# Kernel tuning notes

Hardware: AMD Instinct MI355X
Metric: run time of the kernel (lower is better)

The kernel has to match this reference:

```python
import jax, jax.numpy as jnp
import numpy as np

ALPHA = 9.0
EPS = 2.220446049250313e-16  # sys.float_info.epsilon
N, K = 131072, 256


def setup_inputs() -> dict:
    key = jax.random.key(0)
    k1, k2 = jax.random.split(key)
    latent_view_1 = jax.random.uniform(k1, (N, K), dtype=jnp.float32)
    latent_view_2 = jax.random.uniform(k2, (N, K), dtype=jnp.float32)
    return {"latent_view_1": latent_view_1, "latent_view_2": latent_view_2}


def reference(latent_view_1, latent_view_2):
    # joint: sum_n v1[n,i] * v2[n,j]  == v1^T @ v2  (rank-N GEMM, [k,k] output)
    p_i_j = jnp.einsum('ni,nj->ij', latent_view_1, latent_view_2)
    p_i_j = (p_i_j + p_i_j.T) / 2.0
    p_i_j = p_i_j / jnp.sum(p_i_j)
    p_i = jnp.sum(p_i_j, axis=1, keepdims=True)  # [k,1] marginal
    p_j = jnp.sum(p_i_j, axis=0, keepdims=True)  # [1,k] marginal
    p_i_j = jnp.maximum(p_i_j, EPS)
    p_i = jnp.maximum(p_i, EPS)
    p_j = jnp.maximum(p_j, EPS)
    loss = -p_i_j * (jnp.log(p_i_j)
                     - (ALPHA + 1.0) * jnp.log(p_j)
                     - (ALPHA + 1.0) * jnp.log(p_i))
    return jnp.sum(loss)
```

## Files before the change

kernel.cpp:

```cpp
#include <hip/hip_runtime.h>
#include <hip/hip_bf16.h>

#define KDIM 256
#define NTOT 131072
#define PN   65536
#define NB   256
#define RPB  512
#define CHROWS 16
#define CH   (CHROWS*KDIM)
#define NTL  16

typedef float f32x4 __attribute__((ext_vector_type(4)));
typedef __bf16 bf16x8 __attribute__((ext_vector_type(8)));

__device__ __forceinline__ unsigned short f2bf(float x){
  unsigned u = __float_as_uint(x);
  u += 0x7fffu + ((u >> 16) & 1u);
  return (unsigned short)(u >> 16);
}
__device__ __forceinline__ unsigned pk2(float lo, float hi){
  return (unsigned)f2bf(lo) | ((unsigned)f2bf(hi) << 16);
}
__device__ __forceinline__ float bf2f(unsigned short u){
  return __uint_as_float((unsigned)u << 16);
}
__device__ __forceinline__ int swz(int i){ return (((i >> 1) ^ (i >> 4)) & 7) << 4; }

struct Stage { f32x4 r0, r1; };

__device__ __forceinline__ void stage_load(Stage& s, const float* src, long off){
  s.r0 = *(const f32x4*)(src + off);
  s.r1 = *(const f32x4*)(src + off + KDIM);
}

__device__ __forceinline__ void stage_store(const Stage& s, char* tile, const int* offW){
#pragma unroll
  for (int m = 0; m < 4; ++m)
    *(unsigned*)(tile + offW[m]) = pk2(s.r0[m], s.r1[m]);
}

__device__ __forceinline__ void compute_t(const char* As, const char* Bs,
                                          const int* offA, const int* offB,
                                          f32x4 (&acc)[4][4])
{
  bf16x8 af[4], bfr[4];
#pragma unroll
  for (int m = 0; m < 4; ++m) af[m]  = *(const bf16x8*)(As + offA[m]);
#pragma unroll
  for (int n = 0; n < 4; ++n) bfr[n] = *(const bf16x8*)(Bs + offB[n]);
#pragma unroll
  for (int m = 0; m < 4; ++m)
#pragma unroll
    for (int n = 0; n < 4; ++n)
      acc[m][n] = __builtin_amdgcn_mfma_f32_16x16x32_bf16(af[m], bfr[n], acc[m][n], 0, 0, 0);
}

__device__ __forceinline__ void lds_fence_barrier(){
  __builtin_amdgcn_sched_barrier(0);
  asm volatile("s_waitcnt lgkmcnt(0)");
  __builtin_amdgcn_sched_barrier(0);
  __builtin_amdgcn_s_barrier();
  __builtin_amdgcn_sched_barrier(0);
}

__global__ __launch_bounds__(1024) void k_gemm(const float* __restrict__ v1,
                                               const float* __restrict__ v2,
                                               unsigned short* __restrict__ part)
{
  __shared__ char sm[65536];
  const int t    = threadIdx.x;
  const int b    = blockIdx.x;
  const int lane = t & 63, wid = t >> 6;
  const int di   = lane & 15, g = lane >> 4;
  const int wr   = wid >> 2, wc = wid & 3;
  const int i0   = wr * 64, j0 = wc * 64;

  const int mtx = t >> 9;
  const int p   = (t >> 6) & 7;
  const int q   = t & 63;
  const float* src = (mtx ? v2 : v1) + ((long)b * RPB + 2 * p) * KDIM + 4 * q;
  const int sbase = mtx * 16384;

  int offW0[4], offW1[4], offA[4], offB[4];
#pragma unroll
  for (int m = 0; m < 4; ++m){
    const int i   = 4*q + m;
    const int lin = (i << 6) + (p << 2);
    offW0[m] = sbase + ( lin        ^ swz(i));
    offW1[m] = sbase + ((lin + 32)  ^ swz(i));
  }
#pragma unroll
  for (int m = 0; m < 4; ++m){ int i = i0 + 16*m + di; offA[m] = ((i << 6) + (g << 4)) ^ swz(i); }
#pragma unroll
  for (int n = 0; n < 4; ++n){ int j = j0 + 16*n + di; offB[n] = ((j << 6) + (g << 4)) ^ swz(j); }

  f32x4 acc[4][4];
#pragma unroll
  for (int m = 0; m < 4; ++m)
#pragma unroll
    for (int n = 0; n < 4; ++n){ f32x4 z = {0.f,0.f,0.f,0.f}; acc[m][n] = z; }

  Stage S0, S1;
  stage_load(S0, src, 0L * CH);
  stage_load(S1, src, 1L * CH);
  stage_store(S0, sm, offW0);
  __builtin_amdgcn_sched_barrier(0);
  stage_load(S0, src, 2L * CH);
  __builtin_amdgcn_sched_barrier(0);
  stage_store(S1, sm, offW1);
  __builtin_amdgcn_sched_barrier(0);
  stage_load(S1, src, 3L * CH);
  lds_fence_barrier();

#pragma unroll 2
  for (int it = 0; it < NTL - 2; ++it){
    char* Tc = sm + (it & 1) * 32768;
    char* Tn = sm + ((it + 1) & 1) * 32768;
    stage_store(S0, Tn, offW0);
    __builtin_amdgcn_sched_barrier(0);
    stage_load(S0, src, (long)(2*it + 4) * CH);
    __builtin_amdgcn_sched_barrier(0);
    stage_store(S1, Tn, offW1);
    __builtin_amdgcn_sched_barrier(0);
    stage_load(S1, src, (long)(2*it + 5) * CH);
    __builtin_amdgcn_sched_barrier(0);
    compute_t(Tc, Tc + 16384, offA, offB, acc);
    lds_fence_barrier();
  }

  {
    char* Tc = sm + ((NTL - 2) & 1) * 32768;
    char* Tn = sm + ((NTL - 1) & 1) * 32768;
    stage_store(S0, Tn, offW0);
    stage_store(S1, Tn, offW1);
    __builtin_amdgcn_sched_barrier(0);
    compute_t(Tc, Tc + 16384, offA, offB, acc);
    lds_fence_barrier();
    compute_t(Tn, Tn + 16384, offA, offB, acc);
  }

  unsigned short* op = part + (size_t)b * PN;
#pragma unroll
  for (int m = 0; m < 4; ++m)
#pragma unroll
    for (int n = 0; n < 4; ++n){
      const int i = i0 + 16*m + 4*g;
      const int j = j0 + 16*n + di;
#pragma unroll
      for (int r = 0; r < 4; ++r)
        op[(size_t)(i + r) * KDIM + j] = f2bf(acc[m][n][r]);
    }
}

__global__ __launch_bounds__(1024) void k_reduce(const unsigned short* __restrict__ part,
                                                 float* __restrict__ P,
                                                 float* __restrict__ rsum,
                                                 float* __restrict__ csum)
{
  __shared__ float red[1024];
  const int gr = blockIdx.x;
  const int t  = threadIdx.x;
  const int j  = t & 255, q = t >> 8;
  const int bpq = NB >> 2;
  float s = 0.f;
  const unsigned short* p = part + (size_t)(q * bpq) * PN + gr * KDIM + j;
  for (int b = 0; b < bpq; ++b) s += bf2f(p[(size_t)b * PN]);
  red[t] = s; __syncthreads();
  if (t < 512) red[t] += red[t + 512];
  __syncthreads();
  float v = 0.f;
  if (t < 256){
    v = red[t] + red[t + 256];
    P[gr * KDIM + t] = v;
    atomicAdd(&csum[t], v);
  }
  __syncthreads();
  red[t] = (t < 256) ? v : 0.f;
  __syncthreads();
  for (int st = 128; st > 0; st >>= 1){
    if (t < st) red[t] += red[t + st];
    __syncthreads();
  }
  if (t == 0) rsum[gr] = red[0];
}

__global__ __launch_bounds__(256) void k_marg(const float* __restrict__ rsum,
                                              const float* __restrict__ csum,
                                              float* __restrict__ lm,
                                              float* __restrict__ scal,
                                              float* __restrict__ out)
{
  __shared__ float red[256];
  const int i = threadIdx.x;
  float ri = rsum[i];
  red[i] = ri; __syncthreads();
  for (int st = 128; st > 0; st >>= 1){
    if (i < st) red[i] += red[i + st];
    __syncthreads();
  }
  const float S = red[0];
  const float inv2S = 0.5f / S;
  float mi = (ri + csum[i]) * inv2S;
  mi = fmaxf(mi, 2.220446049250313e-16f);
  lm[i] = logf(mi);
  if (i == 0){ scal[0] = inv2S; out[0] = 0.f; }
}

__global__ __launch_bounds__(256) void k_loss(const float* __restrict__ P,
                                              const float* __restrict__ lm,
                                              const float* __restrict__ scal,
                                              float* __restrict__ out)
{
  __shared__ float red[256];
  const float inv2S = scal[0];
  float acc = 0.f;
  const int base = blockIdx.x * 512;
  for (int e = base + threadIdx.x; e < base + 512; e += 256){
    const int i = e >> 8, j = e & 255;
    float q = (P[i * KDIM + j] + P[j * KDIM + i]) * inv2S;
    q = fmaxf(q, 2.220446049250313e-16f);
    acc += -q * (logf(q) - 10.0f * (lm[i] + lm[j]));
  }
  red[threadIdx.x] = acc; __syncthreads();
  for (int st = 128; st > 0; st >>= 1){
    if (threadIdx.x < st) red[threadIdx.x] += red[threadIdx.x + st];
    __syncthreads();
  }
  if (threadIdx.x == 0) atomicAdd(out, red[0]);
}

extern "C" void kernel_launch(void* const* d_in, const int* in_sizes, int n_in,
                              void* d_out, int out_size, void* d_ws, size_t ws_size,
                              hipStream_t stream) {
  const float* v1 = (const float*)d_in[0];
  const float* v2 = (const float*)d_in[1];
  float* out = (float*)d_out;
  char*  wsc = (char*)d_ws;

  unsigned short* part = (unsigned short*)wsc;
  float* P    = (float*)(wsc + (size_t)NB * PN * 2);
  float* rsum = P + PN;
  float* csum = rsum + 256;
  float* lm   = csum + 256;
  float* scal = lm + 256;

  hipMemsetAsync(csum, 0, 256 * sizeof(float), stream);
  k_gemm  <<<NB, 1024, 0, stream>>>(v1, v2, part);
  k_reduce<<<256, 1024, 0, stream>>>(part, P, rsum, csum);
  k_marg  <<<1, 256, 0, stream>>>(rsum, csum, lm, scal, out);
  k_loss  <<<128, 256, 0, stream>>>(P, lm, scal, out);
}
```

Measured before the change: 79.17 us.

## Split GEMM output columns across two 512-thread blocks with packed LDS offsets

The GEMM now launches 512 blocks of 512 threads, each computing a 256x128 half of the output instead of 256 blocks of 1024 threads computing the full 256x256. LDS use per block drops from 64KB to 48KB, and LDS offsets are packed into 16-bit pairs to save registers, with launch bounds asking for four blocks per CU. The goal is higher occupancy and better latency hiding. The cost is that every v1 row chunk is loaded twice, once per column half, and the reduce kernel's indexing changes to match the new partial-sum layout.

```diff
diff --git a/kernel.cpp b/kernel.cpp
--- a/kernel.cpp
+++ b/kernel.cpp
@@ -4,11 +4,12 @@
 #define KDIM 256
 #define NTOT 131072
 #define PN   65536
-#define NB   256
+#define NGB  512
 #define RPB  512
-#define CHROWS 16
-#define CH   (CHROWS*KDIM)
 #define NTL  16
+#define CH   (32*KDIM)
+#define PSZ  32768
+#define BUFB 24576
 
 typedef float f32x4 __attribute__((ext_vector_type(4)));
 typedef __bf16 bf16x8 __attribute__((ext_vector_type(8)));
@@ -33,26 +34,28 @@
   s.r1 = *(const f32x4*)(src + off + KDIM);
 }
 
-__device__ __forceinline__ void stage_store(const Stage& s, char* tile, const int* offW){
+__device__ __forceinline__ void stage_store(const Stage& s, char* T, const unsigned* pW, int x){
+#pragma unroll
+  for (int m = 0; m < 4; ++m){
+    const int off = (int)((pW[m >> 1] >> ((m & 1) * 16)) & 0xffffu) ^ x;
+    *(unsigned*)(T + off) = pk2(s.r0[m], s.r1[m]);
+  }
+}
+
+__device__ __forceinline__ void compute_t(const char* T, const unsigned* pFa,
+                                          const unsigned* pFb, f32x4 (&acc)[4][4])
+{
+  bf16x8 af[4];
 #pragma unroll
   for (int m = 0; m < 4; ++m)
-    *(unsigned*)(tile + offW[m]) = pk2(s.r0[m], s.r1[m]);
-}
-
-__device__ __forceinline__ void compute_t(const char* As, const char* Bs,
-                                          const int* offA, const int* offB,
-                                          f32x4 (&acc)[4][4])
-{
-  bf16x8 af[4], bfr[4];
-#pragma unroll
-  for (int m = 0; m < 4; ++m) af[m]  = *(const bf16x8*)(As + offA[m]);
-#pragma unroll
-  for (int n = 0; n < 4; ++n) bfr[n] = *(const bf16x8*)(Bs + offB[n]);
-#pragma unroll
-  for (int m = 0; m < 4; ++m)
-#pragma unroll
-    for (int n = 0; n < 4; ++n)
-      acc[m][n] = __builtin_amdgcn_mfma_f32_16x16x32_bf16(af[m], bfr[n], acc[m][n], 0, 0, 0);
+    af[m] = *(const bf16x8*)(T + ((pFa[m >> 1] >> ((m & 1) * 16)) & 0xffffu));
+#pragma unroll
+  for (int n = 0; n < 4; ++n){
+    bf16x8 bf = *(const bf16x8*)(T + ((pFb[n >> 1] >> ((n & 1) * 16)) & 0xffffu));
+#pragma unroll
+    for (int m = 0; m < 4; ++m)
+      acc[m][n] = __builtin_amdgcn_mfma_f32_16x16x32_bf16(af[m], bf, acc[m][n], 0, 0, 0);
+  }
 }
 
 __device__ __forceinline__ void lds_fence_barrier(){
@@ -63,36 +66,42 @@
   __builtin_amdgcn_sched_barrier(0);
 }
 
-__global__ __launch_bounds__(1024) void k_gemm(const float* __restrict__ v1,
-                                               const float* __restrict__ v2,
-                                               unsigned short* __restrict__ part)
-{
-  __shared__ char sm[65536];
+__global__ __launch_bounds__(512, 4) void k_gemm(const float* __restrict__ v1,
+                                                 const float* __restrict__ v2,
+                                                 unsigned short* __restrict__ part)
+{
+  __shared__ char sm[2 * BUFB];
   const int t    = threadIdx.x;
   const int b    = blockIdx.x;
+  const int r    = b & 255, h = b >> 8;
   const int lane = t & 63, wid = t >> 6;
   const int di   = lane & 15, g = lane >> 4;
-  const int wr   = wid >> 2, wc = wid & 3;
-  const int i0   = wr * 64, j0 = wc * 64;
-
-  const int mtx = t >> 9;
-  const int p   = (t >> 6) & 7;
-  const int q   = t & 63;
-  const float* src = (mtx ? v2 : v1) + ((long)b * RPB + 2 * p) * KDIM + 4 * q;
-  const int sbase = mtx * 16384;
-
-  int offW0[4], offW1[4], offA[4], offB[4];
-#pragma unroll
-  for (int m = 0; m < 4; ++m){
-    const int i   = 4*q + m;
-    const int lin = (i << 6) + (p << 2);
-    offW0[m] = sbase + ( lin        ^ swz(i));
-    offW1[m] = sbase + ((lin + 32)  ^ swz(i));
-  }
-#pragma unroll
-  for (int m = 0; m < 4; ++m){ int i = i0 + 16*m + di; offA[m] = ((i << 6) + (g << 4)) ^ swz(i); }
-#pragma unroll
-  for (int n = 0; n < 4; ++n){ int j = j0 + 16*n + di; offB[n] = ((j << 6) + (g << 4)) ^ swz(j); }
+  const int i0   = (wid >> 1) * 64;
+  const int j0l  = (wid & 1) * 64;
+
+  const int rpA = t >> 6, qA = t & 63;
+  const int rpB = t >> 5, qB = t & 31;
+  const long rowBase = (long)r * RPB;
+  const float* pA  = v1 + (rowBase + 2 * rpA) * KDIM + 4 * qA;
+  const float* pA2 = pA + 16 * KDIM;
+  const float* pB  = v2 + (rowBase + 2 * rpB) * KDIM + h * 128 + 4 * qB;
+
+  unsigned pWa[2], pWb[2], pFa[2], pFb[2];
+#pragma unroll
+  for (int m = 0; m < 4; m += 2){
+    const int i1 = 4*qA + m, i2 = i1 + 1;
+    pWa[m>>1] = (unsigned)((((i1 << 6) + (rpA << 2)) ^ swz(i1)) & 0xffff)
+              | ((unsigned)((((i2 << 6) + (rpA << 2)) ^ swz(i2)) & 0xffff) << 16);
+    const int j1 = 4*qB + m, j2 = j1 + 1;
+    pWb[m>>1] = (unsigned)((16384 + (((j1 << 6) + (rpB << 2)) ^ swz(j1))) & 0xffff)
+              | ((unsigned)((16384 + (((j2 << 6) + (rpB << 2)) ^ swz(j2))) & 0xffff) << 16);
+    const int ia = i0 + 16*m + di, ib = i0 + 16*(m+1) + di;
+    pFa[m>>1] = (unsigned)((((ia << 6) + (g << 4)) ^ swz(ia)) & 0xffff)
+              | ((unsigned)((((ib << 6) + (g << 4)) ^ swz(ib)) & 0xffff) << 16);
+    const int ja = j0l + 16*m + di, jb = j0l + 16*(m+1) + di;
+    pFb[m>>1] = (unsigned)((16384 + (((ja << 6) + (g << 4)) ^ swz(ja))) & 0xffff)
+              | ((unsigned)((16384 + (((jb << 6) + (g << 4)) ^ swz(jb))) & 0xffff) << 16);
+  }
 
   f32x4 acc[4][4];
 #pragma unroll
@@ -100,55 +109,61 @@
 #pragma unroll
     for (int n = 0; n < 4; ++n){ f32x4 z = {0.f,0.f,0.f,0.f}; acc[m][n] = z; }
 
-  Stage S0, S1;
-  stage_load(S0, src, 0L * CH);
-  stage_load(S1, src, 1L * CH);
-  stage_store(S0, sm, offW0);
-  __builtin_amdgcn_sched_barrier(0);
-  stage_load(S0, src, 2L * CH);
-  __builtin_amdgcn_sched_barrier(0);
-  stage_store(S1, sm, offW1);
-  __builtin_amdgcn_sched_barrier(0);
-  stage_load(S1, src, 3L * CH);
+  Stage A0, A1, B0;
+  stage_load(A0, pA,  0);
+  stage_load(A1, pA2, 0);
+  stage_load(B0, pB,  0);
+  stage_store(A0, sm, pWa, 0);
+  stage_store(A1, sm, pWa, 32);
+  stage_store(B0, sm, pWb, 0);
+  __builtin_amdgcn_sched_barrier(0);
+  stage_load(A0, pA,  CH);
+  stage_load(A1, pA2, CH);
+  stage_load(B0, pB,  CH);
   lds_fence_barrier();
 
 #pragma unroll 2
   for (int it = 0; it < NTL - 2; ++it){
-    char* Tc = sm + (it & 1) * 32768;
-    char* Tn = sm + ((it + 1) & 1) * 32768;
-    stage_store(S0, Tn, offW0);
-    __builtin_amdgcn_sched_barrier(0);
-    stage_load(S0, src, (long)(2*it + 4) * CH);
-    __builtin_amdgcn_sched_barrier(0);
-    stage_store(S1, Tn, offW1);
-    __builtin_amdgcn_sched_barrier(0);
-    stage_load(S1, src, (long)(2*it + 5) * CH);
-    __builtin_amdgcn_sched_barrier(0);
-    compute_t(Tc, Tc + 16384, offA, offB, acc);
+    char* Tc = sm + (it & 1) * BUFB;
+    char* Tn = sm + ((it + 1) & 1) * BUFB;
+    stage_store(A0, Tn, pWa, 0);
+    __builtin_amdgcn_sched_barrier(0);
+    stage_load(A0, pA,  (long)(it + 2) * CH);
+    __builtin_amdgcn_sched_barrier(0);
+    stage_store(A1, Tn, pWa, 32);
+    __builtin_amdgcn_sched_barrier(0);
+    stage_load(A1, pA2, (long)(it + 2) * CH);
+    __builtin_amdgcn_sched_barrier(0);
+    stage_store(B0, Tn, pWb, 0);
+    __builtin_amdgcn_sched_barrier(0);
+    stage_load(B0, pB,  (long)(it + 2) * CH);
+    __builtin_amdgcn_sched_barrier(0);
+    compute_t(Tc, pFa, pFb, acc);
     lds_fence_barrier();
   }
 
   {
-    char* Tc = sm + ((NTL - 2) & 1) * 32768;
-    char* Tn = sm + ((NTL - 1) & 1) * 32768;
-    stage_store(S0, Tn, offW0);
-    stage_store(S1, Tn, offW1);
-    __builtin_amdgcn_sched_barrier(0);
-    compute_t(Tc, Tc + 16384, offA, offB, acc);
+    char* Tc = sm + ((NTL - 2) & 1) * BUFB;
+    char* Tn = sm + ((NTL - 1) & 1) * BUFB;
+    stage_store(A0, Tn, pWa, 0);
+    stage_store(A1, Tn, pWa, 32);
+    stage_store(B0, Tn, pWb, 0);
+    __builtin_amdgcn_sched_barrier(0);
+    compute_t(Tc, pFa, pFb, acc);
     lds_fence_barrier();
-    compute_t(Tn, Tn + 16384, offA, offB, acc);
-  }
-
-  unsigned short* op = part + (size_t)b * PN;
+    compute_t(Tn, pFa, pFb, acc);
+  }
+
+  unsigned short* op = part + (size_t)b * PSZ;
 #pragma unroll
   for (int m = 0; m < 4; ++m)
 #pragma unroll
     for (int n = 0; n < 4; ++n){
-      const int i = i0 + 16*m + 4*g;
-      const int j = j0 + 16*n + di;
-#pragma unroll
-      for (int r = 0; r < 4; ++r)
-        op[(size_t)(i + r) * KDIM + j] = f2bf(acc[m][n][r]);
+      const int i  = i0 + 16*m + 4*g;
+      const int jl = j0l + 16*n + di;
+#pragma unroll
+      for (int rr = 0; rr < 4; ++rr)
+        op[(size_t)(i + rr) * 128 + jl] = f2bf(acc[m][n][rr]);
     }
 }
 
@@ -161,10 +176,10 @@
   const int gr = blockIdx.x;
   const int t  = threadIdx.x;
   const int j  = t & 255, q = t >> 8;
-  const int bpq = NB >> 2;
+  const int hh = j >> 7, jl = j & 127;
   float s = 0.f;
-  const unsigned short* p = part + (size_t)(q * bpq) * PN + gr * KDIM + j;
-  for (int b = 0; b < bpq; ++b) s += bf2f(p[(size_t)b * PN]);
+  const unsigned short* p = part + (size_t)(hh * 256 + q * 64) * PSZ + gr * 128 + jl;
+  for (int k = 0; k < 64; ++k) s += bf2f(p[(size_t)k * PSZ]);
   red[t] = s; __syncthreads();
   if (t < 512) red[t] += red[t + 512];
   __syncthreads();
@@ -238,14 +253,14 @@
   char*  wsc = (char*)d_ws;
 
   unsigned short* part = (unsigned short*)wsc;
-  float* P    = (float*)(wsc + (size_t)NB * PN * 2);
+  float* P    = (float*)(wsc + (size_t)NGB * PSZ * 2);
   float* rsum = P + PN;
   float* csum = rsum + 256;
   float* lm   = csum + 256;
   float* scal = lm + 256;
 
   hipMemsetAsync(csum, 0, 256 * sizeof(float), stream);
-  k_gemm  <<<NB, 1024, 0, stream>>>(v1, v2, part);
+  k_gemm  <<<NGB, 512, 0, stream>>>(v1, v2, part);
   k_reduce<<<256, 1024, 0, stream>>>(part, P, rsum, csum);
   k_marg  <<<1, 256, 0, stream>>>(rsum, csum, lm, scal, out);
   k_loss  <<<128, 256, 0, stream>>>(P, lm, scal, out);
```

Result: slower. 141.6 us (+78.9%).
